# Performance work log

Hardware: AMD Instinct MI355X
Metric: run time of the kernel (lower is better)

Reference implementation:

```python
import jax, jax.numpy as jnp
import numpy as np

H = 128        # hidden_dim
HEADS = 4      # conv1 heads
NTYPE = 50     # node_type_num
MZN = 32       # model_zoo_num
MAXN = 64      # max_node_num
B = 16         # outer batch
G = B * MZN    # num graphs = 512
N = G * MAXN   # total nodes = 32768
E = N * 8      # edges = 262144


def layer_norm(x, g, b):
    mu = x.mean(-1, keepdims=True)
    var = ((x - mu) ** 2).mean(-1, keepdims=True)
    return (x - mu) / jnp.sqrt(var + 1e-6) * g + b


def gat_conv(x, src, dst, W, a_src, a_dst, bias):
    # PyG GATConv: lin (no bias) -> per-edge LeakyReLU(0.2) scores with
    # self-loops -> segment softmax over dst -> scatter-sum, concat heads + bias.
    n = x.shape[0]
    heads, c = a_src.shape
    xp = (x @ W).reshape(n, heads, c)              # [N,heads,c]
    al_s = (xp * a_src).sum(-1)                    # [N,heads]
    al_d = (xp * a_dst).sum(-1)                    # [N,heads]
    loop = jnp.arange(n)
    s = jnp.concatenate([src, loop])               # add self-loops
    d = jnp.concatenate([dst, loop])
    e = jax.nn.leaky_relu(al_s[s] + al_d[d], 0.2)  # [E+N,heads]
    m = jax.ops.segment_max(e, d, num_segments=n)
    ex = jnp.exp(e - m[d])
    denom = jax.ops.segment_sum(ex, d, num_segments=n)
    alpha = ex / denom[d]                          # segment softmax
    msg = xp[s] * alpha[:, :, None]                # [E+N,heads,c]
    out = jax.ops.segment_sum(msg, d, num_segments=n)
    return out.reshape(n, heads * c) + bias


def setup_inputs() -> dict:
    key = jax.random.key(0)
    ks = jax.random.split(key, 32)
    def rn(k, shape, s=0.05):
        return jax.random.normal(k, shape, jnp.float32) * s
    inp = {
        "t": jax.random.normal(ks[0], (G, 768), jnp.float32),
        "v": jax.random.normal(ks[1], (G, 768), jnp.float32),
        "m_idx": jax.random.randint(ks[2], (N,), 0, NTYPE + 1),
        "edge_index": jax.random.randint(ks[3], (2, E), 0, N),
        "Wt": rn(ks[4], (768, H)), "bt": jnp.zeros((H,), jnp.float32),
        "Wv": rn(ks[5], (768, H)), "bv": jnp.zeros((H,), jnp.float32),
        "emb": rn(ks[6], (NTYPE + 1, H), 1.0),
        "Wnode": rn(ks[7], (H, H)), "bnode": jnp.zeros((H,), jnp.float32),
        "Wstart": rn(ks[8], (2 * H, H)), "bstart": jnp.zeros((H,), jnp.float32),
        "ln_g": jnp.ones((H,), jnp.float32), "ln_b": jnp.zeros((H,), jnp.float32),
        "W1": rn(ks[9], (H, HEADS * H)),
        "a_src1": rn(ks[10], (HEADS, H)), "a_dst1": rn(ks[11], (HEADS, H)),
        "b1": jnp.zeros((HEADS * H,), jnp.float32),
        "W2": rn(ks[12], (HEADS * H, H)),
        "a_src2": rn(ks[13], (1, H)), "a_dst2": rn(ks[14], (1, H)),
        "b2": jnp.zeros((H,), jnp.float32),
        "Wo1": rn(ks[15], (H, H)), "bo1": jnp.zeros((H,), jnp.float32),
        "Wo2": rn(ks[16], (H, 1)), "bo2": jnp.zeros((1,), jnp.float32),
    }
    return inp


def reference(t, v, Wt, bt, Wv, bv, emb, Wnode, bnode, Wstart, bstart, ln_g, ln_b,
              W1, a_src1, a_dst1, b1, W2, a_src2, a_dst2, b2, Wo1, bo1, Wo2, bo2,
              m_idx, edge_index):
    te = t @ Wt + bt                               # [G,H]
    ve = v @ Wv + bv                               # [G,H]
    ne = emb[m_idx].reshape(G, MAXN, H)            # node type embeddings
    ne = ne @ Wnode + bnode
    start = jnp.concatenate([ve, te], axis=-1) @ Wstart + bstart
    ne = ne.at[:, 0].set(start).reshape(N, H)
    x = layer_norm(ne, ln_g, ln_b)
    src, dst = edge_index[0], edge_index[1]
    x = jax.nn.elu(gat_conv(x, src, dst, W1, a_src1, a_dst1, b1))  # [N,4H]
    x = jax.nn.elu(gat_conv(x, src, dst, W2, a_src2, a_dst2, b2))  # [N,H]
    mask = (m_idx >= 1).astype(x.dtype).reshape(G, MAXN, 1)
    pooled = (x.reshape(G, MAXN, H) * mask).sum(1) / mask.sum(1)   # masked mean
    h1 = jax.nn.leaky_relu(pooled.reshape(B, MZN, H) @ Wo1 + bo1, 0.01)
    logits = (h1 @ Wo2 + bo2).reshape(B, MZN)
    return logits
```

## Files before the change

kernel.cpp:

```cpp
#include <hip/hip_runtime.h>
#include <hip/hip_bf16.h>

typedef __hip_bfloat16 bf16;
typedef __attribute__((ext_vector_type(8))) short s8v;
typedef __attribute__((ext_vector_type(4))) float f4v;

#define NN 32768
#define EE 262144
#define GG 512
#define LDW 520

__device__ __forceinline__ float2 unpk(unsigned u) {
  float2 r;
  r.x = __uint_as_float(u << 16);
  r.y = __uint_as_float(u & 0xffff0000u);
  return r;
}
__device__ __forceinline__ unsigned pk(float x, float y) {
  union { bf16 h[2]; unsigned u; } p;
  p.h[0] = __float2bfloat16(x);
  p.h[1] = __float2bfloat16(y);
  return p.u;
}
__device__ __forceinline__ short f2bf_bits(float x) {
  bf16 h = __float2bfloat16(x);
  return *reinterpret_cast<short*>(&h);
}
__device__ __forceinline__ float wred_sum(float v) {
#pragma unroll
  for (int o = 32; o; o >>= 1) v += __shfl_xor(v, o, 64);
  return v;
}

__device__ __forceinline__ void packB_one(const float* W, int N, int K, int id, s8v* Bp) {
  int lane = id & 63;
  int tmp = id >> 6;
  int ksteps = K >> 5;
  int ks = tmp % ksteps;
  int nt = tmp / ksteps;
  int n = nt * 16 + (lane & 15);
  int kbase = ks * 32 + (lane >> 4) * 8;
  s8v r;
#pragma unroll
  for (int j = 0; j < 8; j++) r[j] = f2bf_bits(W[(size_t)(kbase + j) * N + n]);
  Bp[id] = r;
}

__global__ __launch_bounds__(256) void prep_kernel(
    const int* __restrict__ dst, int* __restrict__ indeg,
    const float* __restrict__ W1, s8v* __restrict__ Bp1,
    const float* __restrict__ W2, s8v* __restrict__ Bp2,
    const float* __restrict__ a_src1, const float* __restrict__ a_dst1,
    float* __restrict__ ws1, float* __restrict__ wd1,
    const float* __restrict__ emb, const float* __restrict__ Wnode,
    const float* __restrict__ bnode, bf16* __restrict__ emb2_b,
    const float* __restrict__ Wv, const float* __restrict__ Wt,
    const float* __restrict__ Ws,
    const float* __restrict__ bv, const float* __restrict__ bt,
    const float* __restrict__ bstart,
    float* __restrict__ Wvs, float* __restrict__ Wts,
    float* __restrict__ bs2) {
  int b = blockIdx.x, tid = threadIdx.x;
  if (b < 1024) {
    int e = b * 256 + tid;
    atomicAdd(&indeg[dst[e]], 1);
  } else if (b < 1056) {
    packB_one(W1, 512, 128, (b - 1024) * 256 + tid, Bp1);
  } else if (b < 1088) {
    packB_one(W2, 128, 512, (b - 1056) * 256 + tid, Bp2);
  } else if (b < 1090) {
    int id = (b - 1088) * 256 + tid;
    int h = id >> 7, k = id & 127;
    float s = 0.f, d = 0.f;
    for (int c = 0; c < 128; c++) {
      float w0 = W1[(size_t)k * 512 + h * 128 + c];
      s = fmaf(w0, a_src1[h * 128 + c], s);
      d = fmaf(w0, a_dst1[h * 128 + c], d);
    }
    ws1[id] = s;
    wd1[id] = d;
  } else if (b < 1192) {
    __shared__ float red[256];
    int bb = b - 1090;
    int lo = tid & 63, slice = tid >> 6;
    long oid = (long)bb * 64 + lo;
    bool live = (oid < 51L * 128);
    int m = 0, n = 0;
    if (live) { m = (int)(oid >> 7); n = (int)(oid & 127); }
    float acc = 0.f;
    if (live) {
      const float* Ar = emb + (size_t)m * 128;
      for (int k = slice * 32; k < slice * 32 + 32; k++)
        acc = fmaf(Ar[k], Wnode[(size_t)k * 128 + n], acc);
    }
    red[tid] = acc;
    __syncthreads();
    if (slice == 0 && live) {
      float v = red[lo] + red[64 + lo] + red[128 + lo] + red[192 + lo];
      emb2_b[(size_t)m * 128 + n] = __float2bfloat16(v + bnode[n]);
    }
  } else if (b < 1576) {
    int id = (b - 1192) * 256 + tid;
    bool isT = id >= 49152;
    int o = isT ? id - 49152 : id;
    int k = o >> 6, cp = o & 63, c0 = cp * 2;
    const float* Wrow = (isT ? Wt : Wv) + (size_t)k * 128;
    const float* Wsc = Ws + (isT ? (size_t)128 * 128 : 0);
    float s0 = 0.f, s1 = 0.f;
    for (int j = 0; j < 128; j++) {
      float w = Wrow[j];
      float2 q = *(const float2*)(Wsc + (size_t)j * 128 + c0);
      s0 = fmaf(w, q.x, s0);
      s1 = fmaf(w, q.y, s1);
    }
    float* dp = (isT ? Wts : Wvs) + (size_t)k * 128 + c0;
    dp[0] = s0;
    dp[1] = s1;
  } else {
    if (tid < 128) {
      float s = bstart[tid];
      for (int k = 0; k < 128; k++) {
        s = fmaf(bv[k], Ws[(size_t)k * 128 + tid], s);
        s = fmaf(bt[k], Ws[(size_t)(128 + k) * 128 + tid], s);
      }
      bs2[tid] = s;
    }
  }
}

__global__ __launch_bounds__(1024) void scan_start_kernel(
    const int* __restrict__ indeg, int* __restrict__ off, int* __restrict__ cursor,
    const float* __restrict__ tf, const float* __restrict__ vf,
    const float* __restrict__ Wvs, const float* __restrict__ Wts,
    const float* __restrict__ bs2, bf16* __restrict__ start_b) {
  int t = threadIdx.x;
  if (blockIdx.x == 0) {
    __shared__ int sh[1024];
    int loc[32];
    int s = 0;
    int base = t * 32;
#pragma unroll
    for (int j = 0; j < 32; j++) { loc[j] = indeg[base + j]; s += loc[j]; }
    sh[t] = s;
    __syncthreads();
    for (int d = 1; d < 1024; d <<= 1) {
      int v = (t >= d) ? sh[t - d] : 0;
      __syncthreads();
      sh[t] += v;
      __syncthreads();
    }
    int run = (t == 0) ? 0 : sh[t - 1];
#pragma unroll
    for (int j = 0; j < 32; j++) { off[base + j] = run; cursor[base + j] = run; run += loc[j]; }
    if (t == 1023) off[NN] = run;
    return;
  }
  __shared__ float red[1024];
  int g = blockIdx.x - 1;
  int c = t & 127, slice = t >> 7;
  const float* vrow = vf + (size_t)g * 768;
  const float* trow = tf + (size_t)g * 768;
  float acc = 0.f;
  int k0 = slice * 96;
#pragma unroll 4
  for (int k = k0; k < k0 + 96; k++)
    acc = fmaf(vrow[k], Wvs[(size_t)k * 128 + c], fmaf(trow[k], Wts[(size_t)k * 128 + c], acc));
  red[t] = acc;
  __syncthreads();
  if (t < 512) red[t] += red[t + 512];
  __syncthreads();
  if (t < 256) red[t] += red[t + 256];
  __syncthreads();
  if (t < 128) {
    float s = red[t] + red[t + 128] + bs2[t];
    start_b[(size_t)g * 128 + t] = __float2bfloat16(s);
  }
}

__global__ __launch_bounds__(256) void fill_ln_kernel(
    const int* __restrict__ src, const int* __restrict__ dst,
    int* __restrict__ cursor, int* __restrict__ esrc, int* __restrict__ edst,
    const unsigned* __restrict__ start_b, const unsigned* __restrict__ emb2_b,
    const int* __restrict__ m_idx, const float* __restrict__ lng,
    const float* __restrict__ lnb, const float* __restrict__ ws1,
    const float* __restrict__ wd1, unsigned* __restrict__ x0b,
    float* __restrict__ als, float* __restrict__ ald) {
  int b = blockIdx.x;
  if (b < 1024) {
    int e = b * 256 + threadIdx.x;
    int d = dst[e];
    int p = atomicAdd(&cursor[d], 1);
    esrc[p] = src[e];
    edst[p] = d;
    return;
  }
  int bb = b - 1024;
  int i = bb * 4 + (threadIdx.x >> 6);
  int lane = threadIdx.x & 63;
  int g = i >> 6, n = i & 63;
  const unsigned* row = (n == 0) ? (start_b + (size_t)g * 64) : (emb2_b + (size_t)m_idx[i] * 64);
  float2 v = unpk(row[lane]);
  float mu = wred_sum(v.x + v.y) * (1.f / 128.f);
  float dx = v.x - mu, dy = v.y - mu;
  float var = wred_sum(dx * dx + dy * dy) * (1.f / 128.f);
  float rstd = rsqrtf(var + 1e-6f);
  float2 gg = ((const float2*)lng)[lane];
  float2 bbv = ((const float2*)lnb)[lane];
  float xx = dx * rstd * gg.x + bbv.x;
  float xy = dy * rstd * gg.y + bbv.y;
  x0b[(size_t)i * 64 + lane] = pk(xx, xy);
#pragma unroll
  for (int h = 0; h < 4; h++) {
    float2 s2 = ((const float2*)(ws1 + h * 128))[lane];
    float2 d2 = ((const float2*)(wd1 + h * 128))[lane];
    float ps = wred_sum(xx * s2.x + xy * s2.y);
    float pd = wred_sum(xx * d2.x + xy * d2.y);
    if (lane == 0) { als[i * 4 + h] = ps; ald[i * 4 + h] = pd; }
  }
}

__global__ __launch_bounds__(256) void escore1_kernel(
    const float4* __restrict__ als4, const float4* __restrict__ ald4,
    const int* __restrict__ esrc, const int* __restrict__ edst,
    float4* __restrict__ aw4) {
  int p = blockIdx.x * 256 + threadIdx.x;
  float4 a = als4[esrc[p]];
  float4 d = ald4[edst[p]];
  float v0 = a.x + d.x, v1 = a.y + d.y, v2 = a.z + d.z, v3 = a.w + d.w;
  v0 = v0 > 0.f ? v0 : 0.2f * v0; v1 = v1 > 0.f ? v1 : 0.2f * v1;
  v2 = v2 > 0.f ? v2 : 0.2f * v2; v3 = v3 > 0.f ? v3 : 0.2f * v3;
  aw4[p] = make_float4(__expf(v0), __expf(v1), __expf(v2), __expf(v3));
}

__global__ __launch_bounds__(256, 8) void conv12f_kernel(
    const uint4* __restrict__ x0,
    const float4* __restrict__ aw4,
    const float4* __restrict__ als4, const float4* __restrict__ ald4,
    const int* __restrict__ off, const int* __restrict__ esrc,
    const s8v* __restrict__ Bp1, const float* __restrict__ b1,
    const s8v* __restrict__ Bp2,
    const float* __restrict__ a_src2, const float* __restrict__ a_dst2,
    short* __restrict__ xp2, float* __restrict__ als2, float* __restrict__ ald2) {
  __shared__ short lds[16 * LDW];
  int tid = threadIdx.x;
  int brow = blockIdx.x * 16;
  {
    int c8 = tid & 15, rsub = tid >> 4;
    int i = brow + rsub;
    float4 sa = als4[i], sd = ald4[i];
    float u0 = sa.x + sd.x, u1 = sa.y + sd.y, u2 = sa.z + sd.z, u3 = sa.w + sd.w;
    u0 = u0 > 0.f ? u0 : 0.2f * u0; u1 = u1 > 0.f ? u1 : 0.2f * u1;
    u2 = u2 > 0.f ? u2 : 0.2f * u2; u3 = u3 > 0.f ? u3 : 0.2f * u3;
    float sw0 = __expf(u0), sw1 = __expf(u1), sw2 = __expf(u2), sw3 = __expf(u3);
    float dn0 = sw0, dn1 = sw1, dn2 = sw2, dn3 = sw3;
    uint4 xv = x0[(size_t)i * 16 + c8];
    float x[8];
    { float2 p0 = unpk(xv.x), p1 = unpk(xv.y), p2 = unpk(xv.z), p3 = unpk(xv.w);
      x[0]=p0.x; x[1]=p0.y; x[2]=p1.x; x[3]=p1.y; x[4]=p2.x; x[5]=p2.y; x[6]=p3.x; x[7]=p3.y; }
    float acc[4][8];
#pragma unroll
    for (int j = 0; j < 8; j++) {
      acc[0][j] = sw0 * x[j]; acc[1][j] = sw1 * x[j];
      acc[2][j] = sw2 * x[j]; acc[3][j] = sw3 * x[j];
    }
    int e0 = off[i], e1 = off[i + 1];
#pragma unroll 1
    for (int e = e0; e < e1; e++) {
      int sA = esrc[e];
      float4 wA = aw4[e];
      uint4 mA = x0[(size_t)sA * 16 + c8];
      float2 q0 = unpk(mA.x), q1 = unpk(mA.y), q2 = unpk(mA.z), q3 = unpk(mA.w);
      float qa[8] = {q0.x, q0.y, q1.x, q1.y, q2.x, q2.y, q3.x, q3.y};
#pragma unroll
      for (int j = 0; j < 8; j++) {
        acc[0][j] = fmaf(wA.x, qa[j], acc[0][j]);
        acc[1][j] = fmaf(wA.y, qa[j], acc[1][j]);
        acc[2][j] = fmaf(wA.z, qa[j], acc[2][j]);
        acc[3][j] = fmaf(wA.w, qa[j], acc[3][j]);
      }
      dn0 += wA.x; dn1 += wA.y; dn2 += wA.z; dn3 += wA.w;
    }
    float ivh[4] = {1.f / dn0, 1.f / dn1, 1.f / dn2, 1.f / dn3};
#pragma unroll
    for (int h = 0; h < 4; h++) {
      uint4 o;
      o.x = pk(acc[h][0] * ivh[h], acc[h][1] * ivh[h]);
      o.y = pk(acc[h][2] * ivh[h], acc[h][3] * ivh[h]);
      o.z = pk(acc[h][4] * ivh[h], acc[h][5] * ivh[h]);
      o.w = pk(acc[h][6] * ivh[h], acc[h][7] * ivh[h]);
      *(uint4*)(lds + rsub * LDW + h * 128 + c8 * 8) = o;
    }
  }
  __syncthreads();
  int wv = tid >> 6, lane = tid & 63, quad = lane >> 4, l16 = lane & 15;
  int arow = l16 * LDW;
  {
    int h = wv;
    f4v acc[8] = {};
#pragma unroll
    for (int ks = 0; ks < 4; ks++) {
      s8v a = *(const s8v*)(lds + arow + h * 128 + ks * 32 + quad * 8);
#pragma unroll
      for (int nt = 0; nt < 8; nt++) {
        s8v bf = Bp1[(size_t)((h * 8 + nt) * 4 + ks) * 64 + lane];
        acc[nt] = __builtin_amdgcn_mfma_f32_16x16x32_bf16(a, bf, acc[nt], 0, 0, 0);
      }
    }
#pragma unroll
    for (int nt = 0; nt < 8; nt++) {
      float bb = b1[h * 128 + nt * 16 + l16];
#pragma unroll
      for (int r = 0; r < 4; r++) {
        float vv = acc[nt][r] + bb;
        vv = vv > 0.f ? vv : (__expf(vv) - 1.f);
        lds[(quad * 4 + r) * LDW + h * 128 + nt * 16 + l16] = f2bf_bits(vv);
      }
    }
  }
  __syncthreads();
  f4v acc2[2] = {};
  for (int ks = 0; ks < 16; ks++) {
    s8v a = *(const s8v*)(lds + arow + ks * 32 + quad * 8);
#pragma unroll
    for (int j = 0; j < 2; j++) {
      int nt = wv * 2 + j;
      s8v bf = Bp2[(size_t)(nt * 16 + ks) * 64 + lane];
      acc2[j] = __builtin_amdgcn_mfma_f32_16x16x32_bf16(a, bf, acc2[j], 0, 0, 0);
    }
  }
  __syncthreads();
#pragma unroll
  for (int j = 0; j < 2; j++) {
    int nt = wv * 2 + j;
#pragma unroll
    for (int r = 0; r < 4; r++)
      lds[(quad * 4 + r) * LDW + nt * 16 + l16] = f2bf_bits(acc2[j][r]);
  }
  __syncthreads();
  float2 as = ((const float2*)a_src2)[lane];
  float2 ad = ((const float2*)a_dst2)[lane];
  for (int r = 0; r < 4; r++) {
    int row = wv * 4 + r;
    float2 x = unpk(*(const unsigned*)(lds + row * LDW + lane * 2));
    float ps = wred_sum(x.x * as.x + x.y * as.y);
    float pd = wred_sum(x.x * ad.x + x.y * ad.y);
    if (lane == 0) { als2[brow + row] = ps; ald2[brow + row] = pd; }
  }
  {
    int row = tid >> 4, c16 = tid & 15;
    uint4 val = *(const uint4*)(lds + row * LDW + c16 * 8);
    *(uint4*)(xp2 + (size_t)(brow + row) * 128 + c16 * 8) = val;
  }
}

__global__ __launch_bounds__(1024, 8) void tail2_kernel(
    const uint4* __restrict__ xp,
    const float* __restrict__ als, const float* __restrict__ ald,
    const int* __restrict__ off, const int* __restrict__ esrc,
    const float* __restrict__ b2, const int* __restrict__ m_idx,
    const float* __restrict__ Wo1, const float* __restrict__ bo1,
    const float* __restrict__ Wo2, const float* __restrict__ bo2,
    float* __restrict__ out) {
  __shared__ float x2t[64 * 132];
  __shared__ float maskf[64];
  __shared__ float pl[128];
  __shared__ float red[1024];
  int g = blockIdx.x, tid = threadIdx.x;
  if (tid < 64) maskf[tid] = (m_idx[g * 64 + tid] >= 1) ? 1.f : 0.f;
  int c8 = tid & 15, rsub = tid >> 4;
  {
    int i = g * 64 + rsub;
    float adi = ald[i];
    float selfSc = als[i] + adi;
    selfSc = selfSc > 0.f ? selfSc : 0.2f * selfSc;
    float sw = __expf(selfSc);
    float dnm = sw;
    uint4 xv = xp[(size_t)i * 16 + c8];
    float2 p0 = unpk(xv.x), p1 = unpk(xv.y), p2 = unpk(xv.z), p3 = unpk(xv.w);
    float a0 = sw * p0.x, a1 = sw * p0.y, a2 = sw * p1.x, a3 = sw * p1.y;
    float a4 = sw * p2.x, a5 = sw * p2.y, a6 = sw * p3.x, a7 = sw * p3.y;
    int s0 = off[i], s1 = off[i + 1];
    int e = s0;
    for (; e + 1 < s1; e += 2) {
      int sA = esrc[e], sB = esrc[e + 1];
      float scA = als[sA] + adi, scB = als[sB] + adi;
      scA = scA > 0.f ? scA : 0.2f * scA;
      scB = scB > 0.f ? scB : 0.2f * scB;
      float wA = __expf(scA), wB = __expf(scB);
      uint4 mA = xp[(size_t)sA * 16 + c8];
      uint4 mB = xp[(size_t)sB * 16 + c8];
      float2 q0 = unpk(mA.x), q1 = unpk(mA.y), q2 = unpk(mA.z), q3 = unpk(mA.w);
      a0 = fmaf(wA, q0.x, a0); a1 = fmaf(wA, q0.y, a1);
      a2 = fmaf(wA, q1.x, a2); a3 = fmaf(wA, q1.y, a3);
      a4 = fmaf(wA, q2.x, a4); a5 = fmaf(wA, q2.y, a5);
      a6 = fmaf(wA, q3.x, a6); a7 = fmaf(wA, q3.y, a7);
      dnm += wA;
      q0 = unpk(mB.x); q1 = unpk(mB.y); q2 = unpk(mB.z); q3 = unpk(mB.w);
      a0 = fmaf(wB, q0.x, a0); a1 = fmaf(wB, q0.y, a1);
      a2 = fmaf(wB, q1.x, a2); a3 = fmaf(wB, q1.y, a3);
      a4 = fmaf(wB, q2.x, a4); a5 = fmaf(wB, q2.y, a5);
      a6 = fmaf(wB, q3.x, a6); a7 = fmaf(wB, q3.y, a7);
      dnm += wB;
    }
    if (e < s1) {
      int sA = esrc[e];
      float scA = als[sA] + adi;
      scA = scA > 0.f ? scA : 0.2f * scA;
      float wA = __expf(scA);
      uint4 mA = xp[(size_t)sA * 16 + c8];
      float2 q0 = unpk(mA.x), q1 = unpk(mA.y), q2 = unpk(mA.z), q3 = unpk(mA.w);
      a0 = fmaf(wA, q0.x, a0); a1 = fmaf(wA, q0.y, a1);
      a2 = fmaf(wA, q1.x, a2); a3 = fmaf(wA, q1.y, a3);
      a4 = fmaf(wA, q2.x, a4); a5 = fmaf(wA, q2.y, a5);
      a6 = fmaf(wA, q3.x, a6); a7 = fmaf(wA, q3.y, a7);
      dnm += wA;
    }
    float ivv = 1.f / dnm;
    float4 bb0 = ((const float4*)b2)[c8 * 2];
    float4 bb1 = ((const float4*)b2)[c8 * 2 + 1];
    a0 = a0 * ivv + bb0.x; a1 = a1 * ivv + bb0.y; a2 = a2 * ivv + bb0.z; a3 = a3 * ivv + bb0.w;
    a4 = a4 * ivv + bb1.x; a5 = a5 * ivv + bb1.y; a6 = a6 * ivv + bb1.z; a7 = a7 * ivv + bb1.w;
    a0 = a0 > 0.f ? a0 : (__expf(a0) - 1.f);
    a1 = a1 > 0.f ? a1 : (__expf(a1) - 1.f);
    a2 = a2 > 0.f ? a2 : (__expf(a2) - 1.f);
    a3 = a3 > 0.f ? a3 : (__expf(a3) - 1.f);
    a4 = a4 > 0.f ? a4 : (__expf(a4) - 1.f);
    a5 = a5 > 0.f ? a5 : (__expf(a5) - 1.f);
    a6 = a6 > 0.f ? a6 : (__expf(a6) - 1.f);
    a7 = a7 > 0.f ? a7 : (__expf(a7) - 1.f);
    float* dp = x2t + rsub * 132 + c8 * 8;
    dp[0] = a0; dp[1] = a1; dp[2] = a2; dp[3] = a3;
    dp[4] = a4; dp[5] = a5; dp[6] = a6; dp[7] = a7;
  }
  __syncthreads();
  int c = tid & 127, q = tid >> 7;
  float pacc = 0.f;
  for (int n = q * 8; n < q * 8 + 8; n++) pacc += maskf[n] * x2t[n * 132 + c];
  red[tid] = pacc;
  __syncthreads();
  float cnt = 0.f;
  for (int n = 0; n < 64; n++) cnt += maskf[n];
  if (q == 0) {
    float s = red[c] + red[c + 128] + red[c + 256] + red[c + 384] +
              red[c + 512] + red[c + 640] + red[c + 768] + red[c + 896];
    pl[c] = s / cnt;
  }
  __syncthreads();
  float hacc = 0.f;
  for (int k = q * 16; k < q * 16 + 16; k++)
    hacc = fmaf(pl[k], Wo1[(size_t)k * 128 + c], hacc);
  red[tid] = hacc;
  __syncthreads();
  if (q == 0) {
    float hh = red[c] + red[c + 128] + red[c + 256] + red[c + 384] +
               red[c + 512] + red[c + 640] + red[c + 768] + red[c + 896] + bo1[c];
    hh = hh > 0.f ? hh : 0.01f * hh;
    red[c] = hh * Wo2[c];
  }
  __syncthreads();
  for (int d = 64; d; d >>= 1) {
    if (tid < d) red[tid] += red[tid + d];
    __syncthreads();
  }
  if (tid == 0) out[g] = red[0] + bo2[0];
}

extern "C" void kernel_launch(void* const* d_in, const int* in_sizes, int n_in, void* d_out,
                              int out_size, void* d_ws, size_t ws_size, hipStream_t stream) {
  (void)n_in; (void)out_size; (void)ws_size;
  bool dict_order = (in_sizes[2] == NN);
  int IM, IE, IF[25];
  if (dict_order) {
    IM = 2; IE = 3;
    const int f[25] = {0, 1, 4, 5, 6, 7, 8, 9, 10, 11, 12, 13, 14, 15, 16, 17, 18,
                       19, 20, 21, 22, 23, 24, 25, 26};
    for (int k = 0; k < 25; k++) IF[k] = f[k];
  } else {
    IM = 25; IE = 26;
    for (int k = 0; k < 25; k++) IF[k] = k;
  }
  const int* m_idx = (const int*)d_in[IM];
  const int* eidx = (const int*)d_in[IE];
  float* out = (float*)d_out;
  const int* e_src = eidx;
  const int* e_dst = eidx + EE;

  const float* t = (const float*)d_in[IF[0]];
  const float* v = (const float*)d_in[IF[1]];
  const float* Wt = (const float*)d_in[IF[2]];     const float* bt = (const float*)d_in[IF[3]];
  const float* Wv = (const float*)d_in[IF[4]];     const float* bv = (const float*)d_in[IF[5]];
  const float* emb = (const float*)d_in[IF[6]];
  const float* Wnode = (const float*)d_in[IF[7]];  const float* bnode = (const float*)d_in[IF[8]];
  const float* Wstart = (const float*)d_in[IF[9]]; const float* bstart = (const float*)d_in[IF[10]];
  const float* ln_g = (const float*)d_in[IF[11]];  const float* ln_b = (const float*)d_in[IF[12]];
  const float* W1 = (const float*)d_in[IF[13]];
  const float* a_src1 = (const float*)d_in[IF[14]]; const float* a_dst1 = (const float*)d_in[IF[15]];
  const float* b1 = (const float*)d_in[IF[16]];
  const float* W2 = (const float*)d_in[IF[17]];
  const float* a_src2 = (const float*)d_in[IF[18]]; const float* a_dst2 = (const float*)d_in[IF[19]];
  const float* b2 = (const float*)d_in[IF[20]];
  const float* Wo1 = (const float*)d_in[IF[21]];   const float* bo1 = (const float*)d_in[IF[22]];
  const float* Wo2 = (const float*)d_in[IF[23]];   const float* bo2 = (const float*)d_in[IF[24]];

  char* w = (char*)d_ws;
  bf16* x0b = (bf16*)w;
  bf16* xp2b = (bf16*)(w + ((size_t)8 << 20));
  size_t so = (size_t)16 << 20;
  bf16* emb2_b = (bf16*)(w + so); so += 51 * 128 * 2 + 256;
  bf16* start_b = (bf16*)(w + so); so += 512 * 128 * 2;
  float* als1 = (float*)(w + so); so += NN * 4 * 4;
  float* ald1 = (float*)(w + so); so += NN * 4 * 4;
  float* als2 = (float*)(w + so); so += NN * 4;
  float* ald2 = (float*)(w + so); so += NN * 4;
  float* aw1 = (float*)(w + so); so += EE * 4 * 4;
  float* ws1 = (float*)(w + so); so += 512 * 4;
  float* wd1 = (float*)(w + so); so += 512 * 4;
  float* Wvs = (float*)(w + so); so += 768 * 128 * 4;
  float* Wts = (float*)(w + so); so += 768 * 128 * 4;
  float* bs2 = (float*)(w + so); so += 512;
  int* indeg = (int*)(w + so); so += NN * 4;
  int* csroff = (int*)(w + so); so += (NN + 1) * 4 + 252;
  int* cursor = (int*)(w + so); so += NN * 4;
  int* esrc = (int*)(w + so); so += EE * 4;
  int* edst = (int*)(w + so); so += EE * 4;
  s8v* Bp1 = (s8v*)(w + so); so += 32 * 4 * 64 * 16;
  s8v* Bp2 = (s8v*)(w + so); so += 8 * 16 * 64 * 16;

  hipMemsetAsync(indeg, 0, NN * 4, stream);
  prep_kernel<<<1577, 256, 0, stream>>>(e_dst, indeg,
      W1, Bp1, W2, Bp2, a_src1, a_dst1, ws1, wd1,
      emb, Wnode, bnode, emb2_b,
      Wv, Wt, Wstart, bv, bt, bstart, Wvs, Wts, bs2);
  scan_start_kernel<<<513, 1024, 0, stream>>>(indeg, csroff, cursor,
      t, v, Wvs, Wts, bs2, start_b);
  fill_ln_kernel<<<9216, 256, 0, stream>>>(e_src, e_dst, cursor, esrc, edst,
      (const unsigned*)start_b, (const unsigned*)emb2_b, m_idx, ln_g, ln_b,
      ws1, wd1, (unsigned*)x0b, als1, ald1);
  escore1_kernel<<<EE / 256, 256, 0, stream>>>((const float4*)als1, (const float4*)ald1,
                                               esrc, edst, (float4*)aw1);
  conv12f_kernel<<<NN / 16, 256, 0, stream>>>((const uint4*)x0b,
      (const float4*)aw1, (const float4*)als1, (const float4*)ald1,
      csroff, esrc, Bp1, b1, Bp2, a_src2, a_dst2, (short*)xp2b, als2, ald2);
  tail2_kernel<<<GG, 1024, 0, stream>>>((const uint4*)xp2b, als2, ald2,
      csroff, esrc, b2, m_idx, Wo1, bo1, Wo2, bo2, out);
}
```

Baseline: 274.8 us.

## Split conv12f work across 512 threads by head pairs and MFMA tiles

The fused conv1 aggregation plus GEMM kernel now launches 512 threads per block instead of 256. Each thread aggregates two heads instead of four, halving its accumulator registers. The MFMA stages split the per-wave output tiles in half, which needs an extra barrier before the ELU write-back. This trades more threads and duplicated gather loads of neighbour features (each source row is now fetched by two thread groups) for lower register pressure and more latency hiding. The launch bounds on conv12f and tail2 also drop the explicit occupancy hint.

```diff
diff --git a/kernel.cpp b/kernel.cpp
--- a/kernel.cpp
+++ b/kernel.cpp
@@ -232,7 +232,7 @@
   aw4[p] = make_float4(__expf(v0), __expf(v1), __expf(v2), __expf(v3));
 }
 
-__global__ __launch_bounds__(256, 8) void conv12f_kernel(
+__global__ __launch_bounds__(512) void conv12f_kernel(
     const uint4* __restrict__ x0,
     const float4* __restrict__ aw4,
     const float4* __restrict__ als4, const float4* __restrict__ ald4,
@@ -245,115 +245,109 @@
   int tid = threadIdx.x;
   int brow = blockIdx.x * 16;
   {
-    int c8 = tid & 15, rsub = tid >> 4;
+    int c8 = tid & 15, hp = (tid >> 4) & 1, rsub = tid >> 5;
     int i = brow + rsub;
     float4 sa = als4[i], sd = ald4[i];
-    float u0 = sa.x + sd.x, u1 = sa.y + sd.y, u2 = sa.z + sd.z, u3 = sa.w + sd.w;
-    u0 = u0 > 0.f ? u0 : 0.2f * u0; u1 = u1 > 0.f ? u1 : 0.2f * u1;
-    u2 = u2 > 0.f ? u2 : 0.2f * u2; u3 = u3 > 0.f ? u3 : 0.2f * u3;
-    float sw0 = __expf(u0), sw1 = __expf(u1), sw2 = __expf(u2), sw3 = __expf(u3);
-    float dn0 = sw0, dn1 = sw1, dn2 = sw2, dn3 = sw3;
+    float u0 = hp ? (sa.z + sd.z) : (sa.x + sd.x);
+    float u1 = hp ? (sa.w + sd.w) : (sa.y + sd.y);
+    u0 = u0 > 0.f ? u0 : 0.2f * u0;
+    u1 = u1 > 0.f ? u1 : 0.2f * u1;
+    float sw0 = __expf(u0), sw1 = __expf(u1);
+    float dn0 = sw0, dn1 = sw1;
     uint4 xv = x0[(size_t)i * 16 + c8];
-    float x[8];
-    { float2 p0 = unpk(xv.x), p1 = unpk(xv.y), p2 = unpk(xv.z), p3 = unpk(xv.w);
-      x[0]=p0.x; x[1]=p0.y; x[2]=p1.x; x[3]=p1.y; x[4]=p2.x; x[5]=p2.y; x[6]=p3.x; x[7]=p3.y; }
-    float acc[4][8];
-#pragma unroll
-    for (int j = 0; j < 8; j++) {
-      acc[0][j] = sw0 * x[j]; acc[1][j] = sw1 * x[j];
-      acc[2][j] = sw2 * x[j]; acc[3][j] = sw3 * x[j];
+    float acc0[8], acc1[8];
+    {
+      float2 p0 = unpk(xv.x), p1 = unpk(xv.y), p2 = unpk(xv.z), p3 = unpk(xv.w);
+      float x0v[8] = {p0.x, p0.y, p1.x, p1.y, p2.x, p2.y, p3.x, p3.y};
+#pragma unroll
+      for (int j = 0; j < 8; j++) { acc0[j] = sw0 * x0v[j]; acc1[j] = sw1 * x0v[j]; }
     }
     int e0 = off[i], e1 = off[i + 1];
-#pragma unroll 1
     for (int e = e0; e < e1; e++) {
       int sA = esrc[e];
-      float4 wA = aw4[e];
+      float2 wA = ((const float2*)aw4)[e * 2 + hp];
       uint4 mA = x0[(size_t)sA * 16 + c8];
       float2 q0 = unpk(mA.x), q1 = unpk(mA.y), q2 = unpk(mA.z), q3 = unpk(mA.w);
-      float qa[8] = {q0.x, q0.y, q1.x, q1.y, q2.x, q2.y, q3.x, q3.y};
+      float q[8] = {q0.x, q0.y, q1.x, q1.y, q2.x, q2.y, q3.x, q3.y};
 #pragma unroll
       for (int j = 0; j < 8; j++) {
-        acc[0][j] = fmaf(wA.x, qa[j], acc[0][j]);
-        acc[1][j] = fmaf(wA.y, qa[j], acc[1][j]);
-        acc[2][j] = fmaf(wA.z, qa[j], acc[2][j]);
-        acc[3][j] = fmaf(wA.w, qa[j], acc[3][j]);
+        acc0[j] = fmaf(wA.x, q[j], acc0[j]);
+        acc1[j] = fmaf(wA.y, q[j], acc1[j]);
       }
-      dn0 += wA.x; dn1 += wA.y; dn2 += wA.z; dn3 += wA.w;
-    }
-    float ivh[4] = {1.f / dn0, 1.f / dn1, 1.f / dn2, 1.f / dn3};
-#pragma unroll
-    for (int h = 0; h < 4; h++) {
-      uint4 o;
-      o.x = pk(acc[h][0] * ivh[h], acc[h][1] * ivh[h]);
-      o.y = pk(acc[h][2] * ivh[h], acc[h][3] * ivh[h]);
-      o.z = pk(acc[h][4] * ivh[h], acc[h][5] * ivh[h]);
-      o.w = pk(acc[h][6] * ivh[h], acc[h][7] * ivh[h]);
-      *(uint4*)(lds + rsub * LDW + h * 128 + c8 * 8) = o;
-    }
+      dn0 += wA.x;
+      dn1 += wA.y;
+    }
+    float iv0 = 1.f / dn0, iv1 = 1.f / dn1;
+    uint4 o;
+    o.x = pk(acc0[0] * iv0, acc0[1] * iv0);
+    o.y = pk(acc0[2] * iv0, acc0[3] * iv0);
+    o.z = pk(acc0[4] * iv0, acc0[5] * iv0);
+    o.w = pk(acc0[6] * iv0, acc0[7] * iv0);
+    *(uint4*)(lds + rsub * LDW + (hp * 2) * 128 + c8 * 8) = o;
+    o.x = pk(acc1[0] * iv1, acc1[1] * iv1);
+    o.y = pk(acc1[2] * iv1, acc1[3] * iv1);
+    o.z = pk(acc1[4] * iv1, acc1[5] * iv1);
+    o.w = pk(acc1[6] * iv1, acc1[7] * iv1);
+    *(uint4*)(lds + rsub * LDW + (hp * 2 + 1) * 128 + c8 * 8) = o;
   }
   __syncthreads();
   int wv = tid >> 6, lane = tid & 63, quad = lane >> 4, l16 = lane & 15;
   int arow = l16 * LDW;
   {
-    int h = wv;
-    f4v acc[8] = {};
+    int h = wv >> 1, half = wv & 1;
+    f4v acc[4] = {};
 #pragma unroll
     for (int ks = 0; ks < 4; ks++) {
       s8v a = *(const s8v*)(lds + arow + h * 128 + ks * 32 + quad * 8);
 #pragma unroll
-      for (int nt = 0; nt < 8; nt++) {
+      for (int j = 0; j < 4; j++) {
+        int nt = half * 4 + j;
         s8v bf = Bp1[(size_t)((h * 8 + nt) * 4 + ks) * 64 + lane];
-        acc[nt] = __builtin_amdgcn_mfma_f32_16x16x32_bf16(a, bf, acc[nt], 0, 0, 0);
+        acc[j] = __builtin_amdgcn_mfma_f32_16x16x32_bf16(a, bf, acc[j], 0, 0, 0);
       }
     }
-#pragma unroll
-    for (int nt = 0; nt < 8; nt++) {
+    __syncthreads();
+#pragma unroll
+    for (int j = 0; j < 4; j++) {
+      int nt = half * 4 + j;
       float bb = b1[h * 128 + nt * 16 + l16];
 #pragma unroll
       for (int r = 0; r < 4; r++) {
-        float vv = acc[nt][r] + bb;
+        float vv = acc[j][r] + bb;
         vv = vv > 0.f ? vv : (__expf(vv) - 1.f);
         lds[(quad * 4 + r) * LDW + h * 128 + nt * 16 + l16] = f2bf_bits(vv);
       }
     }
   }
   __syncthreads();
-  f4v acc2[2] = {};
+  f4v acc2 = {};
   for (int ks = 0; ks < 16; ks++) {
     s8v a = *(const s8v*)(lds + arow + ks * 32 + quad * 8);
-#pragma unroll
-    for (int j = 0; j < 2; j++) {
-      int nt = wv * 2 + j;
-      s8v bf = Bp2[(size_t)(nt * 16 + ks) * 64 + lane];
-      acc2[j] = __builtin_amdgcn_mfma_f32_16x16x32_bf16(a, bf, acc2[j], 0, 0, 0);
-    }
-  }
-  __syncthreads();
-#pragma unroll
-  for (int j = 0; j < 2; j++) {
-    int nt = wv * 2 + j;
-#pragma unroll
-    for (int r = 0; r < 4; r++)
-      lds[(quad * 4 + r) * LDW + nt * 16 + l16] = f2bf_bits(acc2[j][r]);
-  }
+    s8v bf = Bp2[(size_t)(wv * 16 + ks) * 64 + lane];
+    acc2 = __builtin_amdgcn_mfma_f32_16x16x32_bf16(a, bf, acc2, 0, 0, 0);
+  }
+  __syncthreads();
+#pragma unroll
+  for (int r = 0; r < 4; r++)
+    lds[(quad * 4 + r) * LDW + wv * 16 + l16] = f2bf_bits(acc2[r]);
   __syncthreads();
   float2 as = ((const float2*)a_src2)[lane];
   float2 ad = ((const float2*)a_dst2)[lane];
-  for (int r = 0; r < 4; r++) {
-    int row = wv * 4 + r;
+  for (int r = 0; r < 2; r++) {
+    int row = wv * 2 + r;
     float2 x = unpk(*(const unsigned*)(lds + row * LDW + lane * 2));
     float ps = wred_sum(x.x * as.x + x.y * as.y);
     float pd = wred_sum(x.x * ad.x + x.y * ad.y);
     if (lane == 0) { als2[brow + row] = ps; ald2[brow + row] = pd; }
   }
-  {
+  if (tid < 256) {
     int row = tid >> 4, c16 = tid & 15;
     uint4 val = *(const uint4*)(lds + row * LDW + c16 * 8);
     *(uint4*)(xp2 + (size_t)(brow + row) * 128 + c16 * 8) = val;
   }
 }
 
-__global__ __launch_bounds__(1024, 8) void tail2_kernel(
+__global__ __launch_bounds__(1024) void tail2_kernel(
     const uint4* __restrict__ xp,
     const float* __restrict__ als, const float* __restrict__ ald,
     const int* __restrict__ off, const int* __restrict__ esrc,
@@ -538,7 +532,7 @@
       ws1, wd1, (unsigned*)x0b, als1, ald1);
   escore1_kernel<<<EE / 256, 256, 0, stream>>>((const float4*)als1, (const float4*)ald1,
                                                esrc, edst, (float4*)aw1);
-  conv12f_kernel<<<NN / 16, 256, 0, stream>>>((const uint4*)x0b,
+  conv12f_kernel<<<NN / 16, 512, 0, stream>>>((const uint4*)x0b,
       (const float4*)aw1, (const float4*)als1, (const float4*)ald1,
       csroff, esrc, Bp1, b1, Bp2, a_src2, a_dst2, (short*)xp2b, als2, ald2);
   tail2_kernel<<<GG, 1024, 0, stream>>>((const uint4*)xp2b, als2, ald2,
```

Measured after the change: 271.7 us. Within noise of the previous version (-1.1%).
